# Kernel optimization log

Hardware: AMD Instinct MI355X
Metric: run time of the kernel (lower is better)

The kernel has to match this reference:

```python
import jax, jax.numpy as jnp
import numpy as np

H = 16       # num heads
D = 128      # head_dim
R = 64       # d_rope_latent
HID = 2048   # hidden_size
DL = 512     # d_latent
EPS = 1e-6


def _rmsnorm(x, g):
    return x * jax.lax.rsqrt(jnp.mean(x * x, axis=-1, keepdims=True) + EPS) * g


def setup_inputs() -> dict:
    key = jax.random.key(0)
    ks = jax.random.split(key, 8)
    B, S = 2, 2048
    s = 0.02
    return {
        "x":   jax.random.normal(ks[0], (B, S, HID), jnp.float32),
        "Wq":  jax.random.normal(ks[1], (HID, H * D), jnp.float32) * s,
        "Wkv": jax.random.normal(ks[2], (HID, DL), jnp.float32) * s,
        "Wkr": jax.random.normal(ks[3], (DL, H * R), jnp.float32) * s,
        "Wkn": jax.random.normal(ks[4], (DL, H * (D - R)), jnp.float32) * s,
        "Wv":  jax.random.normal(ks[5], (DL, H * D), jnp.float32) * s,
        "Wo":  jax.random.normal(ks[6], (H * D, HID), jnp.float32) * s,
        "gq":  jnp.ones((D,), jnp.float32),
        "gk":  jnp.ones((D,), jnp.float32),
    }


def reference(x, Wq, Wkv, Wkr, Wkn, Wv, Wo, gq, gk):
    B, S, _ = x.shape
    # q projection + per-head RMSNorm
    q = _rmsnorm((x @ Wq).reshape(B, S, H, D), gq)          # [B,S,H,D]
    # low-rank KV latent
    lat = x @ Wkv                                            # [B,S,DL]
    kr = (lat @ Wkr).reshape(B, S, H, R)                     # rope part
    kn = (lat @ Wkn).reshape(B, S, H, D - R)                 # nope part
    # pos_encoding is None in source -> no rotation applied, just concat
    k = _rmsnorm(jnp.concatenate([kr, kn], axis=-1), gk)     # [B,S,H,D]
    v = (lat @ Wv).reshape(B, S, H, D)
    # causal SDPA
    scale = 1.0 / jnp.sqrt(jnp.float32(D))
    scores = jnp.einsum('bqhd,bkhd->bhqk', q, k) * scale     # [B,H,S,S]
    causal = jnp.tril(jnp.ones((S, S), bool))
    scores = jnp.where(causal, scores, jnp.float32(-1e30))
    p = jax.nn.softmax(scores, axis=-1)
    o = jnp.einsum('bhqk,bkhd->bqhd', p, v).reshape(B, S, H * D)
    return o @ Wo
```

## Files before the change

### kernel.cpp

```cpp
#include <hip/hip_runtime.h>
#include <cstdint>
#include <cstddef>

typedef short v8s __attribute__((ext_vector_type(8)));
typedef float v4f __attribute__((ext_vector_type(4)));

__device__ inline float bs2f(short s) {
    return __uint_as_float(((unsigned int)(unsigned short)s) << 16);
}
__device__ inline short f2bs(float f) {
    unsigned int u = __float_as_uint(f);
    unsigned int r = (u + 0x7fffu + ((u >> 16) & 1u)) >> 16;
    return (short)r;
}

#define MFMA(a, b, c) __builtin_amdgcn_mfma_f32_16x16x32_bf16((a), (b), (c), 0, 0, 0)

#define GLOAD_LDS16(g, l)                                                  \
    __builtin_amdgcn_global_load_lds(                                      \
        (const __attribute__((address_space(1))) void*)(g),                \
        (__attribute__((address_space(3))) void*)(l), 16, 0, 0)

__global__ __launch_bounds__(256) void prep(const float* __restrict__ x,
                                            short* __restrict__ xb,
                                            const float* __restrict__ Wq,
                                            const float* __restrict__ Wkv,
                                            const float* __restrict__ Wkr,
                                            const float* __restrict__ Wkn,
                                            const float* __restrict__ Wv,
                                            const float* __restrict__ Wo,
                                            short* __restrict__ WtA,
                                            short* __restrict__ WtB,
                                            short* __restrict__ Wot) {
    int blk = blockIdx.x;
    if (blk < 8192) {
        int i = (blk * 256 + threadIdx.x) * 4;
        float4 v = *(const float4*)(x + i);
        short r[4] = {f2bs(v.x), f2bs(v.y), f2bs(v.z), f2bs(v.w)};
        *(uint2*)(xb + i) = *(const uint2*)r;
        return;
    }
    blk -= 8192;
    const float* W;
    short* Wt;
    int K, N, bx, by;
    if (blk < 4096)      { W = Wq;  Wt = WtA;                      K = 2048; N = 2048; bx = blk & 63; by = blk >> 6; }
    else if (blk < 5120) { blk -= 4096; W = Wkv; Wt = WtA + (size_t)2048 * 2048; K = 2048; N = 512;  bx = blk & 15; by = blk >> 4; }
    else if (blk < 5632) { blk -= 5120; W = Wkr; Wt = WtB;                       K = 512;  N = 1024; bx = blk & 31; by = blk >> 5; }
    else if (blk < 6144) { blk -= 5632; W = Wkn; Wt = WtB + (size_t)1024 * 512;  K = 512;  N = 1024; bx = blk & 31; by = blk >> 5; }
    else if (blk < 7168) { blk -= 6144; W = Wv;  Wt = WtB + (size_t)2048 * 512;  K = 512;  N = 2048; bx = blk & 63; by = blk >> 6; }
    else                 { blk -= 7168; W = Wo;  Wt = Wot;                       K = 2048; N = 2048; bx = blk & 63; by = blk >> 6; }

    __shared__ float tile[32][33];
    const int tx = threadIdx.x & 31, ty = threadIdx.x >> 5;
    const int n0 = bx * 32, k0 = by * 32;
#pragma unroll
    for (int i = 0; i < 32; i += 8) tile[ty + i][tx] = W[(size_t)(k0 + ty + i) * N + n0 + tx];
    __syncthreads();
#pragma unroll
    for (int i = 0; i < 32; i += 8)
        Wt[(size_t)(n0 + ty + i) * K + k0 + tx] = f2bs(tile[tx][ty + i]);
}

__global__ __launch_bounds__(256) void gemm_bt(const short* __restrict__ A,
                                               const short* __restrict__ Bt,
                                               void* __restrict__ C0,
                                               void* __restrict__ C1,
                                               void* __restrict__ C2,
                                               int M, int N, int K, int mode,
                                               const float* __restrict__ g,
                                               float scale) {
    __shared__ short As[2 * 128 * 32];
    __shared__ short Bs[2 * 128 * 32];
    const int tid = threadIdx.x;
    const int lane = tid & 63, wave = tid >> 6;
    const int l16 = lane & 15, quad = lane >> 4;
    const int wm = (wave >> 1) * 64, wn = (wave & 1) * 64;

    const int gx = gridDim.x;
    const int nwg = gx * gridDim.y;
    const int wg = blockIdx.y * gx + blockIdx.x;
    const int cpx = nwg >> 3;
    const int swz = (wg & 7) * cpx + (wg >> 3);
    const int m0 = (swz / gx) * 128, n0 = (swz % gx) * 128;

    const v4f VZ = {0.f, 0.f, 0.f, 0.f};
    v4f acc[4][4];
#pragma unroll
    for (int i = 0; i < 4; i++)
#pragma unroll
        for (int j = 0; j < 4; j++) acc[i][j] = VZ;

    const int r0 = wave * 32 + (lane >> 2);
    const int r1 = r0 + 16;
    const int c0 = ((lane & 3) ^ ((r0 >> 1) & 3)) * 8;
    const int c1 = ((lane & 3) ^ ((r1 >> 1) & 3)) * 8;
    const short* aSrc0 = A + (size_t)(m0 + r0) * K + c0;
    const short* aSrc1 = A + (size_t)(m0 + r1) * K + c1;
    const short* bSrc0 = Bt + (size_t)(n0 + r0) * K + c0;
    const short* bSrc1 = Bt + (size_t)(n0 + r1) * K + c1;
    const int la0 = (wave * 32) * 32, la1 = (wave * 32 + 16) * 32;

    GLOAD_LDS16(aSrc0, &As[la0]);
    GLOAD_LDS16(aSrc1, &As[la1]);
    GLOAD_LDS16(bSrc0, &Bs[la0]);
    GLOAD_LDS16(bSrc1, &Bs[la1]);

    int cur = 0;
    for (int kk = 0; kk < K; kk += 32) {
        __syncthreads();
        __builtin_amdgcn_sched_barrier(0);
        if (kk + 32 < K) {
            const int lo = (cur ^ 1) * 4096;
            GLOAD_LDS16(aSrc0 + kk + 32, &As[lo + la0]);
            GLOAD_LDS16(aSrc1 + kk + 32, &As[lo + la1]);
            GLOAD_LDS16(bSrc0 + kk + 32, &Bs[lo + la0]);
            GLOAD_LDS16(bSrc1 + kk + 32, &Bs[lo + la1]);
        }
        __builtin_amdgcn_sched_barrier(0);

        const int lo = cur * 4096;
        v8s af[4], bfr[4];
#pragma unroll
        for (int t = 0; t < 4; t++) {
            const int ra = wm + t * 16 + l16;
            af[t] = *(const v8s*)(&As[lo + ra * 32 + ((quad ^ ((ra >> 1) & 3)) * 8)]);
        }
#pragma unroll
        for (int t = 0; t < 4; t++) {
            const int rb = wn + t * 16 + l16;
            bfr[t] = *(const v8s*)(&Bs[lo + rb * 32 + ((quad ^ ((rb >> 1) & 3)) * 8)]);
        }
#pragma unroll
        for (int i = 0; i < 4; i++)
#pragma unroll
            for (int j = 0; j < 4; j++) acc[i][j] = MFMA(af[i], bfr[j], acc[i][j]);
        cur ^= 1;
    }

    if (mode == 2) {
        if (n0 < 2048) {
            __syncthreads();
            float* red = (float*)As;
#pragma unroll
            for (int i = 0; i < 4; i++) {
#pragma unroll
                for (int r = 0; r < 4; r++) {
                    float ss2 = 0.f;
#pragma unroll
                    for (int j = 0; j < 4; j++) { float v = acc[i][j][r]; ss2 += v * v; }
#pragma unroll
                    for (int off2 = 1; off2 < 16; off2 <<= 1) ss2 += __shfl_xor(ss2, off2);
                    if (l16 == 0) red[(wm + i * 16 + quad * 4 + r) * 2 + (wn >> 6)] = ss2;
                }
            }
            __syncthreads();
            float gv[4];
#pragma unroll
            for (int j = 0; j < 4; j++) gv[j] = g[wn + j * 16 + l16];
#pragma unroll
            for (int i = 0; i < 4; i++) {
#pragma unroll
                for (int r = 0; r < 4; r++) {
                    const int rl = wm + i * 16 + quad * 4 + r;
                    const float rs =
                        rsqrtf((red[rl * 2] + red[rl * 2 + 1]) * (1.f / 128.f) + 1e-6f) * scale;
#pragma unroll
                    for (int j = 0; j < 4; j++)
                        ((short*)C0)[(size_t)(m0 + rl) * 2048 + n0 + wn + j * 16 + l16] =
                            f2bs(acc[i][j][r] * rs * gv[j]);
                }
            }
        } else {
#pragma unroll
            for (int i = 0; i < 4; i++)
#pragma unroll
                for (int r = 0; r < 4; r++) {
                    const int row = m0 + wm + i * 16 + quad * 4 + r;
#pragma unroll
                    for (int j = 0; j < 4; j++)
                        ((short*)C1)[(size_t)row * 512 + n0 - 2048 + wn + j * 16 + l16] =
                            f2bs(acc[i][j][r]);
                }
        }
        return;
    }

    if (mode == 3 && n0 >= 2048) {
        short* C = (short*)C2;
#pragma unroll
        for (int i = 0; i < 4; i++) {
            const int row = m0 + wm + i * 16 + quad * 4;
            const int bq = row >> 11, s = row & 2047;
            const int kt = s >> 6, key = s & 63;
#pragma unroll
            for (int j = 0; j < 4; j++) {
                const int col = n0 - 2048 + wn + j * 16 + l16;
                const int hh = col >> 7, d = col & 127;
                size_t base = ((size_t)((bq * 16 + hh) * 32 + kt) * 128 + d) * 64 + key;
                short pk[4];
#pragma unroll
                for (int r = 0; r < 4; r++) pk[r] = f2bs(acc[i][j][r]);
                *(uint2*)(C + base) = *(const uint2*)pk;
            }
        }
        return;
    }

    void* Cb = C0;
    int ld = N, coff = 0;
    if (mode == 3) {
        if (n0 < 1024) { Cb = C0; ld = 1024; coff = 0; }
        else           { Cb = C1; ld = 1024; coff = 1024; }
    }
#pragma unroll
    for (int i = 0; i < 4; i++) {
#pragma unroll
        for (int r = 0; r < 4; r++) {
            const int row = m0 + wm + i * 16 + quad * 4 + r;
#pragma unroll
            for (int j = 0; j < 4; j++) {
                const int col = n0 - coff + wn + j * 16 + l16;
                float v = acc[i][j][r];
                if (mode == 1) ((float*)Cb)[(size_t)row * ld + col] = v;
                else ((short*)Cb)[(size_t)row * ld + col] = f2bs(v);
            }
        }
    }
}

__global__ __launch_bounds__(256) void rmsnorm_k(const short* __restrict__ KR,
                                                 const short* __restrict__ KN,
                                                 const float* __restrict__ g,
                                                 short* __restrict__ Y) {
    const int tid = threadIdx.x;
    const int rh = blockIdx.x * 32 + (tid >> 3);
    const int j = tid & 7;
    const size_t ibase = (size_t)blockIdx.x * 2048 + (size_t)tid * 8;
    v8s a = *(const v8s*)(KR + ibase);
    v8s c = *(const v8s*)(KN + ibase);
    float af[8], cf[8];
    float ss = 0.f;
#pragma unroll
    for (int t = 0; t < 8; t++) {
        af[t] = bs2f(a[t]);
        cf[t] = bs2f(c[t]);
        ss += af[t] * af[t] + cf[t] * cf[t];
    }
#pragma unroll
    for (int off = 1; off < 8; off <<= 1) ss += __shfl_xor(ss, off);
    const float rs = rsqrtf(ss * (1.f / 128.f) + 1e-6f);
    const int m = rh >> 4, h = rh & 15;
    const int b = m >> 11, s = m & 2047;
    const size_t obase = ((size_t)((b * 16 + h) * 32 + (s >> 6)) * 64 + (s & 63)) * 128;
    const float* gp = g + j * 8;
    v8s o0, o1;
#pragma unroll
    for (int t = 0; t < 8; t++) {
        o0[t] = f2bs(af[t] * rs * gp[t]);
        o1[t] = f2bs(cf[t] * rs * gp[64 + t]);
    }
    *(v8s*)(Y + obase + j * 8) = o0;
    *(v8s*)(Y + obase + 64 + j * 8) = o1;
}

#define PSTR 72

__global__ __launch_bounds__(256) void flash_attn(const short* __restrict__ Q,
                                                  const short* __restrict__ Kp,
                                                  const short* __restrict__ Vp,
                                                  short* __restrict__ O, int S) {
    __shared__ short Ks[64 * 128];
    __shared__ short Vs[128 * 64];
    __shared__ short Ps[4][16 * PSTR];

    const int lane = threadIdx.x & 63, w = threadIdx.x >> 6;
    const int l16 = lane & 15, quad = lane >> 4;
    const int blk = blockIdx.x;
    const int g = blk >> 3;
    const int bh = (blk & 7) * 4 + (g & 3);
    const int b = bh >> 4, h = bh & 15;
    const int qb = 31 - (g >> 2);
    const int q0 = qb * 64 + w * 16;

    const int koffE = (lane >> 4) * 128 + (((lane & 15) ^ (lane >> 4)) << 3);
    const int koffO = (lane >> 4) * 128 + (((lane & 15) ^ 4 ^ (lane >> 4)) << 3);
    const int voffc = (lane >> 3) * 64 + (((lane & 7) ^ (lane >> 3)) << 3);
    const int swz = (l16 & 7) * 8;

    v8s bq[4];
    {
        const size_t qbase = ((size_t)(b * S + q0 + l16) * 16 + h) * 128;
#pragma unroll
        for (int kc = 0; kc < 4; kc++)
            bq[kc] = *(const v8s*)(Q + qbase + kc * 32 + quad * 8);
    }

    const v4f VZ = {0.f, 0.f, 0.f, 0.f};
    v4f accO[8];
    v4f accL = VZ;
#pragma unroll
    for (int d = 0; d < 8; d++) accO[d] = VZ;

    const short o1 = 0x3F80;
    const v8s vones = {o1, o1, o1, o1, o1, o1, o1, o1};

    const short* const kbh = Kp + (size_t)(bh * 32) * 8192;
    const short* const vbh = Vp + (size_t)(bh * 32) * 8192;

    const int nkt = qb + 1;
    for (int kt = 0; kt < nkt; ++kt) {
        __syncthreads();
        {
            const short* kb = kbh + (size_t)kt * 8192;
            const short* vb = vbh + (size_t)kt * 8192;
            const int c0 = w * 4;
            GLOAD_LDS16(kb + (c0 + 0) * 512 + koffE, Ks + (c0 + 0) * 512);
            GLOAD_LDS16(kb + (c0 + 1) * 512 + koffO, Ks + (c0 + 1) * 512);
            GLOAD_LDS16(kb + (c0 + 2) * 512 + koffE, Ks + (c0 + 2) * 512);
            GLOAD_LDS16(kb + (c0 + 3) * 512 + koffO, Ks + (c0 + 3) * 512);
            GLOAD_LDS16(vb + (c0 + 0) * 512 + voffc, Vs + (c0 + 0) * 512);
            GLOAD_LDS16(vb + (c0 + 1) * 512 + voffc, Vs + (c0 + 1) * 512);
            GLOAD_LDS16(vb + (c0 + 2) * 512 + voffc, Vs + (c0 + 2) * 512);
            GLOAD_LDS16(vb + (c0 + 3) * 512 + voffc, Vs + (c0 + 3) * 512);
        }
        __syncthreads();

        v4f sc[4];
        __builtin_amdgcn_s_setprio(1);
#pragma unroll
        for (int nt = 0; nt < 4; nt++) {
            v8s ak[4];
            const int krow = (nt * 16 + l16) * 128;
#pragma unroll
            for (int kc = 0; kc < 4; kc++)
                ak[kc] = *(const v8s*)(Ks + krow + ((quad * 8 + kc * 32) ^ swz));
            v4f s = VZ;
#pragma unroll
            for (int kc = 0; kc < 4; kc++) s = MFMA(ak[kc], bq[kc], s);
            sc[nt] = s;
        }
        __builtin_amdgcn_s_setprio(0);

        if (kt == nkt - 1) {
            const int qrow = q0 + l16;
            const int k0 = kt * 64;
#pragma unroll
            for (int nt = 0; nt < 4; nt++)
#pragma unroll
                for (int r = 0; r < 4; r++)
                    if (k0 + nt * 16 + quad * 4 + r > qrow) sc[nt][r] = -1e30f;
        }

#pragma unroll
        for (int nt = 0; nt < 4; nt++) {
            short pk[4];
#pragma unroll
            for (int r = 0; r < 4; r++) {
                float p = exp2f(sc[nt][r] - 20.f);
                pk[r] = (short)(__float_as_uint(p) >> 16);
            }
            *(uint2*)(&Ps[w][l16 * PSTR + nt * 16 + quad * 4]) = *(const uint2*)pk;
        }

        v8s ap[2];
#pragma unroll
        for (int kc2 = 0; kc2 < 2; kc2++)
            ap[kc2] = *(const v8s*)(&Ps[w][l16 * PSTR + kc2 * 32 + quad * 8]);
        __builtin_amdgcn_s_setprio(1);
#pragma unroll
        for (int dt = 0; dt < 8; dt++) {
            const int vrow = (dt * 16 + l16) * 64;
#pragma unroll
            for (int kc2 = 0; kc2 < 2; kc2++) {
                v8s bv = *(const v8s*)(Vs + vrow + ((quad * 8 + kc2 * 32) ^ swz));
                accO[dt] = MFMA(ap[kc2], bv, accO[dt]);
            }
        }
#pragma unroll
        for (int kc2 = 0; kc2 < 2; kc2++) accL = MFMA(ap[kc2], vones, accL);
        __builtin_amdgcn_s_setprio(0);
    }

#pragma unroll
    for (int r = 0; r < 4; r++) {
        const int rl = quad * 4 + r;
        const int qg = q0 + rl;
        const float inv = 1.f / accL[r];
        const size_t obase = ((size_t)(b * S + qg) * 16 + h) * 128;
#pragma unroll
        for (int dt = 0; dt < 8; dt++)
            O[obase + dt * 16 + l16] = f2bs(accO[dt][r] * inv);
    }
}

extern "C" void kernel_launch(void* const* d_in, const int* in_sizes, int n_in,
                              void* d_out, int out_size, void* d_ws, size_t ws_size,
                              hipStream_t stream) {
    (void)in_sizes; (void)n_in; (void)out_size; (void)ws_size;
    const float* x   = (const float*)d_in[0];
    const float* Wq  = (const float*)d_in[1];
    const float* Wkv = (const float*)d_in[2];
    const float* Wkr = (const float*)d_in[3];
    const float* Wkn = (const float*)d_in[4];
    const float* Wv  = (const float*)d_in[5];
    const float* Wo  = (const float*)d_in[6];
    const float* gq  = (const float*)d_in[7];
    const float* gk  = (const float*)d_in[8];

    const int B = 2, S = 2048, HID = 2048;
    const int M = B * S;

    char* ws = (char*)d_ws;
    size_t off = 0;
    auto alloc = [&](size_t bytes) {
        char* p = ws + off;
        off += (bytes + 255) & ~(size_t)255;
        return p;
    };
    short* xb   = (short*)alloc((size_t)M * HID * 2);
    short* WtA  = (short*)alloc((size_t)2560 * 2048 * 2);
    short* WtB  = (short*)alloc((size_t)4096 * 512 * 2);
    short* Wot  = (short*)alloc((size_t)2048 * 2048 * 2);
    short* qb   = (short*)alloc((size_t)M * 2048 * 2);
    short* lat  = (short*)alloc((size_t)M * 512 * 2);
    short* krr  = (short*)alloc((size_t)M * 1024 * 2);
    short* knr  = (short*)alloc((size_t)M * 1024 * 2);
    short* Kp   = (short*)alloc((size_t)M * 2048 * 2);
    short* Vp   = (short*)alloc((size_t)M * 2048 * 2);
    short* ob   = (short*)alloc((size_t)M * 2048 * 2);

    prep<<<19456, 256, 0, stream>>>(x, xb, Wq, Wkv, Wkr, Wkn, Wv, Wo, WtA, WtB, Wot);

    gemm_bt<<<dim3(2560 / 128, M / 128), 256, 0, stream>>>(
        xb, WtA, qb, lat, nullptr, M, 2560, 2048, 2, gq,
        0.08838834764831845f * 1.4426950408889634f);

    gemm_bt<<<dim3(4096 / 128, M / 128), 256, 0, stream>>>(
        lat, WtB, krr, knr, Vp, M, 4096, 512, 3, nullptr, 0.f);
    rmsnorm_k<<<(M * 16) / 32, 256, 0, stream>>>(krr, knr, gk, Kp);

    flash_attn<<<dim3(1024), 256, 0, stream>>>(qb, Kp, Vp, ob, S);

    gemm_bt<<<dim3(2048 / 128, M / 128), 256, 0, stream>>>(
        ob, Wot, d_out, nullptr, nullptr, M, 2048, 2048, 1, nullptr, 0.f);
}
```

Baseline: 330.4 us.

## Double-buffer K/V tiles in LDS to prefetch next tile during compute

```diff
diff --git a/kernel.cpp b/kernel.cpp
--- a/kernel.cpp
+++ b/kernel.cpp
@@ -270,8 +270,8 @@
                                                   const short* __restrict__ Kp,
                                                   const short* __restrict__ Vp,
                                                   short* __restrict__ O, int S) {
-    __shared__ short Ks[64 * 128];
-    __shared__ short Vs[128 * 64];
+    __shared__ short Ks[2][64 * 128];
+    __shared__ short Vs[2][128 * 64];
     __shared__ short Ps[4][16 * PSTR];
 
     const int lane = threadIdx.x & 63, w = threadIdx.x >> 6;
@@ -288,6 +288,10 @@
     const int voffc = (lane >> 3) * 64 + (((lane & 7) ^ (lane >> 3)) << 3);
     const int swz = (l16 & 7) * 8;
 
+    const short* const kbh = Kp + (size_t)(bh * 32) * 8192;
+    const short* const vbh = Vp + (size_t)(bh * 32) * 8192;
+    const int c0 = w * 4;
+
     v8s bq[4];
     {
         const size_t qbase = ((size_t)(b * S + q0 + l16) * 16 + h) * 128;
@@ -305,26 +309,43 @@
     const short o1 = 0x3F80;
     const v8s vones = {o1, o1, o1, o1, o1, o1, o1, o1};
 
-    const short* const kbh = Kp + (size_t)(bh * 32) * 8192;
-    const short* const vbh = Vp + (size_t)(bh * 32) * 8192;
-
     const int nkt = qb + 1;
+
+    {
+        const short* kb = kbh;
+        const short* vb = vbh;
+        GLOAD_LDS16(kb + (c0 + 0) * 512 + koffE, &Ks[0][(c0 + 0) * 512]);
+        GLOAD_LDS16(kb + (c0 + 1) * 512 + koffO, &Ks[0][(c0 + 1) * 512]);
+        GLOAD_LDS16(kb + (c0 + 2) * 512 + koffE, &Ks[0][(c0 + 2) * 512]);
+        GLOAD_LDS16(kb + (c0 + 3) * 512 + koffO, &Ks[0][(c0 + 3) * 512]);
+        GLOAD_LDS16(vb + (c0 + 0) * 512 + voffc, &Vs[0][(c0 + 0) * 512]);
+        GLOAD_LDS16(vb + (c0 + 1) * 512 + voffc, &Vs[0][(c0 + 1) * 512]);
+        GLOAD_LDS16(vb + (c0 + 2) * 512 + voffc, &Vs[0][(c0 + 2) * 512]);
+        GLOAD_LDS16(vb + (c0 + 3) * 512 + voffc, &Vs[0][(c0 + 3) * 512]);
+    }
+
+    int cur = 0;
     for (int kt = 0; kt < nkt; ++kt) {
         __syncthreads();
-        {
-            const short* kb = kbh + (size_t)kt * 8192;
-            const short* vb = vbh + (size_t)kt * 8192;
-            const int c0 = w * 4;
-            GLOAD_LDS16(kb + (c0 + 0) * 512 + koffE, Ks + (c0 + 0) * 512);
-            GLOAD_LDS16(kb + (c0 + 1) * 512 + koffO, Ks + (c0 + 1) * 512);
-            GLOAD_LDS16(kb + (c0 + 2) * 512 + koffE, Ks + (c0 + 2) * 512);
-            GLOAD_LDS16(kb + (c0 + 3) * 512 + koffO, Ks + (c0 + 3) * 512);
-            GLOAD_LDS16(vb + (c0 + 0) * 512 + voffc, Vs + (c0 + 0) * 512);
-            GLOAD_LDS16(vb + (c0 + 1) * 512 + voffc, Vs + (c0 + 1) * 512);
-            GLOAD_LDS16(vb + (c0 + 2) * 512 + voffc, Vs + (c0 + 2) * 512);
-            GLOAD_LDS16(vb + (c0 + 3) * 512 + voffc, Vs + (c0 + 3) * 512);
-        }
-        __syncthreads();
+        __builtin_amdgcn_sched_barrier(0);
+        if (kt + 1 < nkt) {
+            const short* kb = kbh + (size_t)(kt + 1) * 8192;
+            const short* vb = vbh + (size_t)(kt + 1) * 8192;
+            short* ksd = &Ks[cur ^ 1][0];
+            short* vsd = &Vs[cur ^ 1][0];
+            GLOAD_LDS16(kb + (c0 + 0) * 512 + koffE, ksd + (c0 + 0) * 512);
+            GLOAD_LDS16(kb + (c0 + 1) * 512 + koffO, ksd + (c0 + 1) * 512);
+            GLOAD_LDS16(kb + (c0 + 2) * 512 + koffE, ksd + (c0 + 2) * 512);
+            GLOAD_LDS16(kb + (c0 + 3) * 512 + koffO, ksd + (c0 + 3) * 512);
+            GLOAD_LDS16(vb + (c0 + 0) * 512 + voffc, vsd + (c0 + 0) * 512);
+            GLOAD_LDS16(vb + (c0 + 1) * 512 + voffc, vsd + (c0 + 1) * 512);
+            GLOAD_LDS16(vb + (c0 + 2) * 512 + voffc, vsd + (c0 + 2) * 512);
+            GLOAD_LDS16(vb + (c0 + 3) * 512 + voffc, vsd + (c0 + 3) * 512);
+        }
+        __builtin_amdgcn_sched_barrier(0);
+
+        const short* const ksr = &Ks[cur][0];
+        const short* const vsr = &Vs[cur][0];
 
         v4f sc[4];
         __builtin_amdgcn_s_setprio(1);
@@ -334,7 +355,7 @@
             const int krow = (nt * 16 + l16) * 128;
 #pragma unroll
             for (int kc = 0; kc < 4; kc++)
-                ak[kc] = *(const v8s*)(Ks + krow + ((quad * 8 + kc * 32) ^ swz));
+                ak[kc] = *(const v8s*)(ksr + krow + ((quad * 8 + kc * 32) ^ swz));
             v4f s = VZ;
 #pragma unroll
             for (int kc = 0; kc < 4; kc++) s = MFMA(ak[kc], bq[kc], s);
@@ -373,13 +394,14 @@
             const int vrow = (dt * 16 + l16) * 64;
 #pragma unroll
             for (int kc2 = 0; kc2 < 2; kc2++) {
-                v8s bv = *(const v8s*)(Vs + vrow + ((quad * 8 + kc2 * 32) ^ swz));
+                v8s bv = *(const v8s*)(vsr + vrow + ((quad * 8 + kc2 * 32) ^ swz));
                 accO[dt] = MFMA(ap[kc2], bv, accO[dt]);
             }
         }
 #pragma unroll
         for (int kc2 = 0; kc2 < 2; kc2++) accL = MFMA(ap[kc2], vones, accL);
         __builtin_amdgcn_s_setprio(0);
+        cur ^= 1;
     }
 
 #pragma unroll
```

Result: no change. 329.1 us, median of 3 (-0.4%).

## Switch flash attention to 32x32x16 MFMA with split-K waves and register-resident P

Applied to the files above, without the earlier changes.

```diff
diff --git a/kernel.cpp b/kernel.cpp
--- a/kernel.cpp
+++ b/kernel.cpp
@@ -4,6 +4,7 @@
 
 typedef short v8s __attribute__((ext_vector_type(8)));
 typedef float v4f __attribute__((ext_vector_type(4)));
+typedef float v16f __attribute__((ext_vector_type(16)));
 
 __device__ inline float bs2f(short s) {
     return __uint_as_float(((unsigned int)(unsigned short)s) << 16);
@@ -13,8 +14,12 @@
     unsigned int r = (u + 0x7fffu + ((u >> 16) & 1u)) >> 16;
     return (short)r;
 }
+__device__ inline unsigned pkbf(float a, float b) {
+    return (__float_as_uint(a) >> 16) | (__float_as_uint(b) & 0xffff0000u);
+}
 
 #define MFMA(a, b, c) __builtin_amdgcn_mfma_f32_16x16x32_bf16((a), (b), (c), 0, 0, 0)
+#define MFMA32(a, b, c) __builtin_amdgcn_mfma_f32_32x32x16_bf16((a), (b), (c), 0, 0, 0)
 
 #define GLOAD_LDS16(g, l)                                                  \
     __builtin_amdgcn_global_load_lds(                                      \
@@ -264,49 +269,46 @@
     *(v8s*)(Y + obase + 64 + j * 8) = o1;
 }
 
-#define PSTR 72
-
-__global__ __launch_bounds__(256) void flash_attn(const short* __restrict__ Q,
-                                                  const short* __restrict__ Kp,
-                                                  const short* __restrict__ Vp,
-                                                  short* __restrict__ O, int S) {
+__global__ __launch_bounds__(256, 3) void flash_attn(const short* __restrict__ Q,
+                                                     const short* __restrict__ Kp,
+                                                     const short* __restrict__ Vp,
+                                                     short* __restrict__ O, int S) {
     __shared__ short Ks[64 * 128];
     __shared__ short Vs[128 * 64];
-    __shared__ short Ps[4][16 * PSTR];
+    __shared__ float Lb[64];
 
     const int lane = threadIdx.x & 63, w = threadIdx.x >> 6;
-    const int l16 = lane & 15, quad = lane >> 4;
+    const int l32 = lane & 31, hl = lane >> 5, l8 = lane & 7;
+    const int qg = w & 1, kg = w >> 1;
     const int blk = blockIdx.x;
     const int g = blk >> 3;
     const int bh = (blk & 7) * 4 + (g & 3);
-    const int b = bh >> 4, h = bh & 15;
+    const int b = bh >> 4, hd = bh & 15;
     const int qb = 31 - (g >> 2);
-    const int q0 = qb * 64 + w * 16;
+    const int q0w = qb * 64 + qg * 32;
 
     const int koffE = (lane >> 4) * 128 + (((lane & 15) ^ (lane >> 4)) << 3);
     const int koffO = (lane >> 4) * 128 + (((lane & 15) ^ 4 ^ (lane >> 4)) << 3);
     const int voffc = (lane >> 3) * 64 + (((lane & 7) ^ (lane >> 3)) << 3);
-    const int swz = (l16 & 7) * 8;
-
-    v8s bq[4];
+
+    v8s bq[8];
     {
-        const size_t qbase = ((size_t)(b * S + q0 + l16) * 16 + h) * 128;
-#pragma unroll
-        for (int kc = 0; kc < 4; kc++)
-            bq[kc] = *(const v8s*)(Q + qbase + kc * 32 + quad * 8);
-    }
-
-    const v4f VZ = {0.f, 0.f, 0.f, 0.f};
-    v4f accO[8];
-    v4f accL = VZ;
-#pragma unroll
-    for (int d = 0; d < 8; d++) accO[d] = VZ;
-
-    const short o1 = 0x3F80;
-    const v8s vones = {o1, o1, o1, o1, o1, o1, o1, o1};
+        const size_t qbase = ((size_t)(b * S + q0w + l32) * 16 + hd) * 128;
+#pragma unroll
+        for (int dc = 0; dc < 8; dc++)
+            bq[dc] = *(const v8s*)(Q + qbase + dc * 16 + hl * 8);
+    }
+
+    v16f accO[4];
+#pragma unroll
+    for (int dg = 0; dg < 4; dg++)
+#pragma unroll
+        for (int i = 0; i < 16; i++) accO[dg][i] = 0.f;
+    float Lacc = 0.f;
 
     const short* const kbh = Kp + (size_t)(bh * 32) * 8192;
     const short* const vbh = Vp + (size_t)(bh * 32) * 8192;
+    const int c0 = w * 4;
 
     const int nkt = qb + 1;
     for (int kt = 0; kt < nkt; ++kt) {
@@ -314,7 +316,6 @@
         {
             const short* kb = kbh + (size_t)kt * 8192;
             const short* vb = vbh + (size_t)kt * 8192;
-            const int c0 = w * 4;
             GLOAD_LDS16(kb + (c0 + 0) * 512 + koffE, Ks + (c0 + 0) * 512);
             GLOAD_LDS16(kb + (c0 + 1) * 512 + koffO, Ks + (c0 + 1) * 512);
             GLOAD_LDS16(kb + (c0 + 2) * 512 + koffE, Ks + (c0 + 2) * 512);
@@ -326,71 +327,90 @@
         }
         __syncthreads();
 
-        v4f sc[4];
+        v16f acc2;
+#pragma unroll
+        for (int i = 0; i < 16; i++) acc2[i] = 0.f;
         __builtin_amdgcn_s_setprio(1);
 #pragma unroll
-        for (int nt = 0; nt < 4; nt++) {
-            v8s ak[4];
-            const int krow = (nt * 16 + l16) * 128;
-#pragma unroll
-            for (int kc = 0; kc < 4; kc++)
-                ak[kc] = *(const v8s*)(Ks + krow + ((quad * 8 + kc * 32) ^ swz));
-            v4f s = VZ;
-#pragma unroll
-            for (int kc = 0; kc < 4; kc++) s = MFMA(ak[kc], bq[kc], s);
-            sc[nt] = s;
+        for (int dc = 0; dc < 8; dc++) {
+            const int row = kg * 32 + l32;
+            const v8s ak =
+                *(const v8s*)(Ks + row * 128 + ((dc * 16 + hl * 8) ^ (l8 << 3)));
+            acc2 = MFMA32(ak, bq[dc], acc2);
         }
         __builtin_amdgcn_s_setprio(0);
 
-        if (kt == nkt - 1) {
-            const int qrow = q0 + l16;
-            const int k0 = kt * 64;
-#pragma unroll
-            for (int nt = 0; nt < 4; nt++)
-#pragma unroll
-                for (int r = 0; r < 4; r++)
-                    if (k0 + nt * 16 + quad * 4 + r > qrow) sc[nt][r] = -1e30f;
-        }
-
-#pragma unroll
-        for (int nt = 0; nt < 4; nt++) {
-            short pk[4];
-#pragma unroll
-            for (int r = 0; r < 4; r++) {
-                float p = exp2f(sc[nt][r] - 20.f);
-                pk[r] = (short)(__float_as_uint(p) >> 16);
-            }
-            *(uint2*)(&Ps[w][l16 * PSTR + nt * 16 + quad * 4]) = *(const uint2*)pk;
-        }
-
-        v8s ap[2];
-#pragma unroll
-        for (int kc2 = 0; kc2 < 2; kc2++)
-            ap[kc2] = *(const v8s*)(&Ps[w][l16 * PSTR + kc2 * 32 + quad * 8]);
-        __builtin_amdgcn_s_setprio(1);
-#pragma unroll
-        for (int dt = 0; dt < 8; dt++) {
-            const int vrow = (dt * 16 + l16) * 64;
-#pragma unroll
-            for (int kc2 = 0; kc2 < 2; kc2++) {
-                v8s bv = *(const v8s*)(Vs + vrow + ((quad * 8 + kc2 * 32) ^ swz));
-                accO[dt] = MFMA(ap[kc2], bv, accO[dt]);
-            }
-        }
-#pragma unroll
-        for (int kc2 = 0; kc2 < 2; kc2++) accL = MFMA(ap[kc2], vones, accL);
-        __builtin_amdgcn_s_setprio(0);
-    }
-
-#pragma unroll
-    for (int r = 0; r < 4; r++) {
-        const int rl = quad * 4 + r;
-        const int qg = q0 + rl;
-        const float inv = 1.f / accL[r];
-        const size_t obase = ((size_t)(b * S + qg) * 16 + h) * 128;
-#pragma unroll
-        for (int dt = 0; dt < 8; dt++)
-            O[obase + dt * 16 + l16] = f2bs(accO[dt][r] * inv);
+        float p[16];
+        const int qglob = q0w + l32;
+        const int kbase = kt * 64 + kg * 32 + 4 * hl;
+#pragma unroll
+        for (int r = 0; r < 16; r++) {
+            float s = acc2[r];
+            if (kt == nkt - 1) {
+                const int key = kbase + (r & 3) + 8 * (r >> 2);
+                if (key > qglob) s = -1e30f;
+            }
+            const float pv = exp2f(s - 20.f);
+            p[r] = pv;
+            Lacc += pv;
+        }
+
+#pragma unroll
+        for (int kcl = 0; kcl < 2; kcl++) {
+            const int rb = kcl * 8;
+            const unsigned qL0 = pkbf(p[rb + 0], p[rb + 1]);
+            const unsigned qL1 = pkbf(p[rb + 2], p[rb + 3]);
+            const unsigned qH0 = pkbf(p[rb + 4], p[rb + 5]);
+            const unsigned qH1 = pkbf(p[rb + 6], p[rb + 7]);
+            const unsigned s0 = hl ? qL0 : qH0;
+            const unsigned s1 = hl ? qL1 : qH1;
+            const unsigned r0 = (unsigned)__shfl_xor((int)s0, 32);
+            const unsigned r1 = (unsigned)__shfl_xor((int)s1, 32);
+            int4 fi = {(int)(hl ? r0 : qL0), (int)(hl ? r1 : qL1),
+                       (int)(hl ? qH0 : r0), (int)(hl ? qH1 : r1)};
+            const v8s pa = *(const v8s*)&fi;
+
+            __builtin_amdgcn_s_setprio(1);
+#pragma unroll
+            for (int dg = 0; dg < 4; dg++) {
+                const int d = dg * 32 + l32;
+                const v8s bv = *(const v8s*)(
+                    Vs + d * 64 + (((kg * 2 + kcl) * 16 + hl * 8) ^ (l8 << 3)));
+                accO[dg] = MFMA32(pa, bv, accO[dg]);
+            }
+            __builtin_amdgcn_s_setprio(0);
+        }
+    }
+
+    const float Ltot = Lacc + __shfl_xor(Lacc, 32);
+
+    __syncthreads();
+    float* dump = (float*)(qg == 0 ? (void*)Ks : (void*)Vs);
+    if (kg) {
+#pragma unroll
+        for (int dg = 0; dg < 4; dg++)
+#pragma unroll
+            for (int r = 0; r < 16; r++) {
+                const int rowidx = (r & 3) + 8 * (r >> 2) + 4 * hl;
+                dump[(dg * 32 + rowidx) * 32 + l32] = accO[dg][r];
+            }
+        if (hl == 0) Lb[qg * 32 + l32] = Ltot;
+    }
+    __syncthreads();
+    if (!kg) {
+        const float Lq = Ltot + Lb[qg * 32 + l32];
+#pragma unroll
+        for (int r = 0; r < 16; r++) {
+            const int rowidx = (r & 3) + 8 * (r >> 2) + 4 * hl;
+            const float inv = 1.f / __shfl(Lq, rowidx);
+            const size_t obase =
+                ((size_t)(b * S + qb * 64 + qg * 32 + rowidx) * 16 + hd) * 128;
+#pragma unroll
+            for (int dg = 0; dg < 4; dg++) {
+                const float v = accO[dg][r] + dump[(dg * 32 + rowidx) * 32 + l32];
+                O[obase + dg * 32 + l32] = f2bs(v * inv);
+            }
+        }
     }
 }
 
```

Result: no change. 334.2 us (+1.2%).
